# Performance work log

Hardware: AMD Instinct MI355X
Metric: run time of the kernel (lower is better)

Reference implementation:

```python
import jax, jax.numpy as jnp
import numpy as np

F_NODE = 32   # node feature dim
E_ATTR = 8    # edge attribute dim
H_OUT = 64    # h_theta output dim


def setup_inputs() -> dict:
    key = jax.random.key(0)
    k1, k2, k3 = jax.random.split(key, 3)
    B, N = 1, 1024
    adjacency = jax.random.randint(k1, (B, N, N), 0, 2, dtype=jnp.int32)
    node_features = jax.random.normal(k2, (B, N, F_NODE), dtype=jnp.float32)
    edge_attributes = jax.random.normal(k3, (B, N, N, E_ATTR), dtype=jnp.float32)
    kW = jax.random.fold_in(key, 7)
    W = jax.random.normal(kW, (2 * F_NODE + E_ATTR, H_OUT), dtype=jnp.float32) * (1.0 / np.sqrt(2 * F_NODE + E_ATTR))
    b = jnp.zeros((H_OUT,), dtype=jnp.float32)
    return {"adjacency": adjacency, "node_features": node_features,
            "edge_attributes": edge_attributes, "W": W, "b": b}


def reference(adjacency, node_features, edge_attributes, W, b):
    # EdgeConvE: per edge (v, v') compute h_theta(concat([x_v, x_v' - x_v, e_vv']))
    # then aggregate over neighbors v' selected by the dense adjacency.
    # Split W along the concat axis so we never materialize the [B,N,N,2F+E] concat:
    # concat @ W = x_v @ W_self + (x_v' - x_v) @ W_diff + e @ W_edge
    F = node_features.shape[-1]
    W_self, W_diff, W_edge = W[:F], W[F:2 * F], W[2 * F:]
    self_term = node_features @ (W_self - W_diff)            # [B,N,H]
    nbr_term = node_features @ W_diff                        # [B,N,H]
    edge_term = jnp.einsum('bvwe,eh->bvwh', edge_attributes, W_edge)  # [B,N,N,H]
    msg = jax.nn.relu(self_term[:, :, None, :] + nbr_term[:, None, :, :] + edge_term + b)
    A = adjacency.astype(msg.dtype)                          # [B,N,N] 0/1 mask
    out = jnp.einsum('bvw,bvwh->bvh', A, msg)                # sum-aggregate over neighbors
    return out
```

## Files before the change

kernel.cpp:

```cpp
#include <hip/hip_runtime.h>
#include <hip/hip_bf16.h>

#define N 1024
#define F 32
#define H 64
#define EA 8

typedef __attribute__((ext_vector_type(8))) short bf16x8;
typedef __attribute__((ext_vector_type(16))) float f32x16;

union FragAB { bf16x8 v; unsigned u[4]; };

__device__ __forceinline__ unsigned pk(float a, float b) {
    union { __hip_bfloat162 h; unsigned u; } c;
    c.h = __float22bfloat162_rn(float2{a, b});
    return c.u;
}

__global__ __launch_bounds__(256) void precompute_terms(
    const float* __restrict__ X, const float* __restrict__ W, const float* __restrict__ b,
    float* __restrict__ sv, float* __restrict__ nb, float* __restrict__ out)
{
    const int lane = threadIdx.x & 63;
    const int wid  = threadIdx.x >> 6;
    const int v    = blockIdx.x * 4 + wid;

    float4 xr[8];
    const float4* xp = (const float4*)(X + (size_t)v * F);
#pragma unroll
    for (int i = 0; i < 8; ++i) xr[i] = xp[i];
    const float* xf = (const float*)xr;

    float s = b[lane];
    float n = 0.f;
#pragma unroll
    for (int f = 0; f < F; ++f) {
        float ws = W[f * H + lane];
        float wd = W[(F + f) * H + lane];
        s = fmaf(xf[f], ws - wd, s);
        n = fmaf(xf[f], wd, n);
    }
    const int idx = v * H + lane;
    sv[idx]  = s;
    nb[idx]  = n;
    out[idx] = 0.f;
}

__global__ __launch_bounds__(256, 4) void edge_mfma(
    const int* __restrict__ A, const float* __restrict__ Edge, const float* __restrict__ W,
    const float* __restrict__ sv, const float* __restrict__ nb, float* __restrict__ out)
{
    const int lane = threadIdx.x & 63;
    const int wid  = threadIdx.x >> 6;
    const int lg   = lane >> 5;
    const int ln   = lane & 31;
    const int wq   = blockIdx.x & 7;
    const int vch  = blockIdx.x >> 3;
    const int wbase = wq * 128 + wid * 32;
    const int vbase = vch * 4;

    __shared__ float part[4][2][4][64];

    const int* ap = A + (size_t)vbase * N + wbase + ln;
    int am[4]; float s0v[4], s1v[4];
#pragma unroll
    for (int vi = 0; vi < 4; ++vi) {
        am[vi]  = ap[(size_t)vi * N];
        s0v[vi] = sv[(size_t)(vbase + vi) * H + ln];
        s1v[vi] = sv[(size_t)(vbase + vi) * H + 32 + ln];
    }

    const float4* ep = (const float4*)(Edge + ((size_t)vbase * N + wbase + ln) * EA);
    float4 eA[2], eB[2];
    eA[0] = ep[0];    eB[0] = ep[1];
    eA[1] = ep[2048]; eB[1] = ep[2049];

    FragAB bfr[2];
#pragma unroll
    for (int half = 0; half < 2; ++half) {
        const int n = half * 32 + ln;
#pragma unroll
        for (int q = 0; q < 4; ++q) {
            unsigned we = pk(W[(2 * F + 2 * q) * H + n], W[(2 * F + 2 * q + 1) * H + n]);
            bfr[half].u[q] = (lg == 0) ? we : 0u;
        }
    }

    f32x16 cnb[2];
#pragma unroll
    for (int half = 0; half < 2; ++half)
#pragma unroll
        for (int r = 0; r < 16; ++r) {
            const int row = (r & 3) + 8 * (r >> 2) + 4 * lg;
            cnb[half][r] = nb[(size_t)(wbase + row) * H + half * 32 + ln];
        }

#pragma unroll
    for (int vi = 0; vi < 4; ++vi) {
        const float4 ca = eA[vi & 1];
        const float4 cb = eB[vi & 1];
        if (vi < 2) {
            eA[vi & 1] = ep[(vi + 2) * 2048];
            eB[vi & 1] = ep[(vi + 2) * 2048 + 1];
        }

        FragAB afr;
        const unsigned mpat = am[vi] ? 0x00003f80u : 0xbf803f80u;
        afr.u[0] = (lg == 0) ? pk(ca.x, ca.y) : mpat;
        afr.u[1] = (lg == 0) ? pk(ca.z, ca.w) : 0u;
        afr.u[2] = (lg == 0) ? pk(cb.x, cb.y) : 0u;
        afr.u[3] = (lg == 0) ? pk(cb.z, cb.w) : 0u;

        FragAB b0 = bfr[0], b1 = bfr[1];
        if (lg) { b0.u[0] = pk(s0v[vi], 1e30f); b1.u[0] = pk(s1v[vi], 1e30f); }

        const f32x16 d0 = __builtin_amdgcn_mfma_f32_32x32x16_bf16(afr.v, b0.v, cnb[0], 0, 0, 0);
        const f32x16 d1 = __builtin_amdgcn_mfma_f32_32x32x16_bf16(afr.v, b1.v, cnb[1], 0, 0, 0);

        float p0 = 0.f, p1 = 0.f;
#pragma unroll
        for (int r = 0; r < 16; ++r) {
            p0 += fmaxf(d0[r], 0.f);
            p1 += fmaxf(d1[r], 0.f);
        }
        part[wid][lg][vi][ln]      = p0;
        part[wid][lg][vi][32 + ln] = p1;
    }

    __syncthreads();
    {
        const int i  = threadIdx.x;
        const int vi = i >> 6, h = i & 63;
        float s = 0.f;
#pragma unroll
        for (int w4 = 0; w4 < 4; ++w4)
#pragma unroll
            for (int g = 0; g < 2; ++g) s += part[w4][g][vi][h];
        atomicAdd(&out[(size_t)(vbase + vi) * H + h], s);
    }
}

extern "C" void kernel_launch(void* const* d_in, const int* in_sizes, int n_in,
                              void* d_out, int out_size, void* d_ws, size_t ws_size,
                              hipStream_t stream) {
    const int*   A    = (const int*)d_in[0];
    const float* X    = (const float*)d_in[1];
    const float* Edge = (const float*)d_in[2];
    const float* W    = (const float*)d_in[3];
    const float* b    = (const float*)d_in[4];
    float* out = (float*)d_out;

    float* sv = (float*)d_ws;
    float* nb = sv + N * H;

    precompute_terms<<<dim3(256), dim3(256), 0, stream>>>(X, W, b, sv, nb, out);
    edge_mfma<<<dim3(2048), dim3(256), 0, stream>>>(A, Edge, W, sv, nb, out);
}
```

Baseline: 90.71 us.

## Fuse node-term precompute into edge kernel via in-block MFMA recomputation

Removes the separate precompute kernel and instead recomputes the neighbor and self projection terms inside each edge block using bf16 MFMA on node features, while the output is zeroed with a memset. This is meant to cut one kernel launch and the global round trip of the intermediate sv/nb buffers. In exchange every block redundantly recomputes these projections, with extra W loads and MFMAs, and these terms are now rounded to bf16, which lowers their precision.

```diff
diff --git a/kernel.cpp b/kernel.cpp
--- a/kernel.cpp
+++ b/kernel.cpp
@@ -17,38 +17,17 @@
     return c.u;
 }
 
-__global__ __launch_bounds__(256) void precompute_terms(
-    const float* __restrict__ X, const float* __restrict__ W, const float* __restrict__ b,
-    float* __restrict__ sv, float* __restrict__ nb, float* __restrict__ out)
-{
-    const int lane = threadIdx.x & 63;
-    const int wid  = threadIdx.x >> 6;
-    const int v    = blockIdx.x * 4 + wid;
-
-    float4 xr[8];
-    const float4* xp = (const float4*)(X + (size_t)v * F);
+__device__ __forceinline__ f32x16 zero16() {
+    f32x16 z;
 #pragma unroll
-    for (int i = 0; i < 8; ++i) xr[i] = xp[i];
-    const float* xf = (const float*)xr;
-
-    float s = b[lane];
-    float n = 0.f;
-#pragma unroll
-    for (int f = 0; f < F; ++f) {
-        float ws = W[f * H + lane];
-        float wd = W[(F + f) * H + lane];
-        s = fmaf(xf[f], ws - wd, s);
-        n = fmaf(xf[f], wd, n);
-    }
-    const int idx = v * H + lane;
-    sv[idx]  = s;
-    nb[idx]  = n;
-    out[idx] = 0.f;
+    for (int r = 0; r < 16; ++r) z[r] = 0.f;
+    return z;
 }
 
-__global__ __launch_bounds__(256, 4) void edge_mfma(
-    const int* __restrict__ A, const float* __restrict__ Edge, const float* __restrict__ W,
-    const float* __restrict__ sv, const float* __restrict__ nb, float* __restrict__ out)
+__global__ __launch_bounds__(256, 4) void edge_fused(
+    const int* __restrict__ A, const float* __restrict__ X,
+    const float* __restrict__ Edge, const float* __restrict__ W,
+    const float* __restrict__ b, float* __restrict__ out)
 {
     const int lane = threadIdx.x & 63;
     const int wid  = threadIdx.x >> 6;
@@ -62,18 +41,68 @@
     __shared__ float part[4][2][4][64];
 
     const int* ap = A + (size_t)vbase * N + wbase + ln;
-    int am[4]; float s0v[4], s1v[4];
+    int am[4];
 #pragma unroll
-    for (int vi = 0; vi < 4; ++vi) {
-        am[vi]  = ap[(size_t)vi * N];
-        s0v[vi] = sv[(size_t)(vbase + vi) * H + ln];
-        s1v[vi] = sv[(size_t)(vbase + vi) * H + 32 + ln];
-    }
+    for (int vi = 0; vi < 4; ++vi) am[vi] = ap[(size_t)vi * N];
 
     const float4* ep = (const float4*)(Edge + ((size_t)vbase * N + wbase + ln) * EA);
     float4 eA[2], eB[2];
     eA[0] = ep[0];    eB[0] = ep[1];
     eA[1] = ep[2048]; eB[1] = ep[2049];
+
+    FragAB aw[2], av[2];
+    {
+        const float* xw = X + (size_t)(wbase + ln) * F;
+        const float* xv = X + (size_t)(vbase + (ln & 3)) * F;
+#pragma unroll
+        for (int s = 0; s < 2; ++s) {
+            const int k0 = s * 16 + lg * 8;
+            const float4 w0 = *(const float4*)(xw + k0);
+            const float4 w1 = *(const float4*)(xw + k0 + 4);
+            aw[s].u[0] = pk(w0.x, w0.y); aw[s].u[1] = pk(w0.z, w0.w);
+            aw[s].u[2] = pk(w1.x, w1.y); aw[s].u[3] = pk(w1.z, w1.w);
+            const float4 v0 = *(const float4*)(xv + k0);
+            const float4 v1 = *(const float4*)(xv + k0 + 4);
+            av[s].u[0] = pk(v0.x, v0.y); av[s].u[1] = pk(v0.z, v0.w);
+            av[s].u[2] = pk(v1.x, v1.y); av[s].u[3] = pk(v1.z, v1.w);
+        }
+    }
+
+    f32x16 cnb[2];
+    unsigned sq0[4], sq1[4];
+    {
+#pragma unroll
+        for (int half = 0; half < 2; ++half) {
+            const int n = half * 32 + ln;
+            FragAB bwd[2], bsd[2];
+#pragma unroll
+            for (int s = 0; s < 2; ++s) {
+                const int k0 = s * 16 + lg * 8;
+#pragma unroll
+                for (int q = 0; q < 4; ++q) {
+                    const float wd0 = W[(F + k0 + 2 * q) * H + n];
+                    const float wd1 = W[(F + k0 + 2 * q + 1) * H + n];
+                    const float ws0 = W[(k0 + 2 * q) * H + n];
+                    const float ws1 = W[(k0 + 2 * q + 1) * H + n];
+                    bwd[s].u[q] = pk(wd0, wd1);
+                    bsd[s].u[q] = pk(ws0 - wd0, ws1 - wd1);
+                }
+            }
+            f32x16 c = zero16();
+            c = __builtin_amdgcn_mfma_f32_32x32x16_bf16(aw[0].v, bwd[0].v, c, 0, 0, 0);
+            c = __builtin_amdgcn_mfma_f32_32x32x16_bf16(aw[1].v, bwd[1].v, c, 0, 0, 0);
+            cnb[half] = c;
+            f32x16 sD = zero16();
+            sD = __builtin_amdgcn_mfma_f32_32x32x16_bf16(av[0].v, bsd[0].v, sD, 0, 0, 0);
+            sD = __builtin_amdgcn_mfma_f32_32x32x16_bf16(av[1].v, bsd[1].v, sD, 0, 0, 0);
+            const float bb = b[n];
+#pragma unroll
+            for (int vi = 0; vi < 4; ++vi) {
+                const unsigned p = pk(sD[vi] + bb, 1e30f);
+                if (half) sq1[vi] = p; else sq0[vi] = p;
+            }
+        }
+    }
 
     FragAB bfr[2];
 #pragma unroll
@@ -85,15 +114,6 @@
             bfr[half].u[q] = (lg == 0) ? we : 0u;
         }
     }
-
-    f32x16 cnb[2];
-#pragma unroll
-    for (int half = 0; half < 2; ++half)
-#pragma unroll
-        for (int r = 0; r < 16; ++r) {
-            const int row = (r & 3) + 8 * (r >> 2) + 4 * lg;
-            cnb[half][r] = nb[(size_t)(wbase + row) * H + half * 32 + ln];
-        }
 
 #pragma unroll
     for (int vi = 0; vi < 4; ++vi) {
@@ -112,7 +132,7 @@
         afr.u[3] = (lg == 0) ? pk(cb.z, cb.w) : 0u;
 
         FragAB b0 = bfr[0], b1 = bfr[1];
-        if (lg) { b0.u[0] = pk(s0v[vi], 1e30f); b1.u[0] = pk(s1v[vi], 1e30f); }
+        if (lg) { b0.u[0] = sq0[vi]; b1.u[0] = sq1[vi]; }
 
         const f32x16 d0 = __builtin_amdgcn_mfma_f32_32x32x16_bf16(afr.v, b0.v, cnb[0], 0, 0, 0);
         const f32x16 d1 = __builtin_amdgcn_mfma_f32_32x32x16_bf16(afr.v, b1.v, cnb[1], 0, 0, 0);
@@ -150,9 +170,6 @@
     const float* b    = (const float*)d_in[4];
     float* out = (float*)d_out;
 
-    float* sv = (float*)d_ws;
-    float* nb = sv + N * H;
-
-    precompute_terms<<<dim3(256), dim3(256), 0, stream>>>(X, W, b, sv, nb, out);
-    edge_mfma<<<dim3(2048), dim3(256), 0, stream>>>(A, Edge, W, sv, nb, out);
+    hipMemsetAsync(out, 0, (size_t)out_size * sizeof(float), stream);
+    edge_fused<<<dim3(2048), dim3(256), 0, stream>>>(A, X, Edge, W, b, out);
 }
```

Result: slower. 96.39 us (+6.3%).
